# Kernel optimization log

Hardware: AMD Instinct MI355X
Metric: run time of the kernel (lower is better)

The kernel has to match this reference:

```python
import jax, jax.numpy as jnp
import numpy as np

D_MODEL = 1024
N_HEADS = 16
D_HEAD = D_MODEL // N_HEADS          # 64
ROT_DIM = D_HEAD // 2                # 32, rotary dim (lucidrains dim arg)
THETA = 10000.0
BATCH, SEQ = 4, 4096


def _rope(t):
    """lucidrains rotate_queries_or_keys with seq_dim=-2, applied to t of shape (H,B,dh,S).
    Positions run along the dh axis (size D_HEAD); rotation touches only the first
    ROT_DIM entries of the last axis (S); the rest passes through unchanged."""
    inv_freq = 1.0 / (THETA ** (jnp.arange(0, ROT_DIM, 2, dtype=jnp.float32) / ROT_DIM))  # (ROT_DIM//2,)
    pos = jnp.arange(D_HEAD, dtype=jnp.float32)                                           # (dh,)
    freqs = pos[:, None] * inv_freq[None, :]                                              # (dh, ROT_DIM//2)
    freqs = jnp.repeat(freqs, 2, axis=-1)                                                 # (dh, ROT_DIM) interleaved f0,f0,f1,f1
    cos, sin = jnp.cos(freqs), jnp.sin(freqs)                                             # broadcast over (H,B,dh,ROT_DIM)
    t_rot, t_pass = t[..., :ROT_DIM], t[..., ROT_DIM:]
    x1, x2 = t_rot[..., 0::2], t_rot[..., 1::2]
    rot_half = jnp.stack((-x2, x1), axis=-1).reshape(t_rot.shape)                         # rotate_half (adjacent pairs)
    t_rot = t_rot * cos + rot_half * sin
    return jnp.concatenate([t_rot, t_pass], axis=-1)


def setup_inputs() -> dict:
    key = jax.random.key(0)
    k1, k2, k3 = jax.random.split(key, 3)
    x = jax.random.normal(k1, (BATCH, SEQ, D_MODEL), jnp.float32)
    W = jax.random.normal(k2, (3 * D_MODEL, D_MODEL), jnp.float32) * (D_MODEL ** -0.5)  # torch Linear weight layout
    b = jax.random.normal(k3, (3 * D_MODEL,), jnp.float32) * 0.01
    return {"x": x, "W": W, "b": b}


def reference(x, W, b):
    B, S, _ = x.shape
    qkv = x @ W.T + b                                            # (B,S,3D)
    qkv = qkv.reshape(B, S, N_HEADS, 3 * D_HEAD).transpose(2, 0, 3, 1)  # (H,B,3dh,S)
    q, k, v = jnp.split(qkv, 3, axis=-2)                         # each (H,B,dh,S)
    q = _rope(q)
    k = _rope(k)
    scale = D_HEAD ** -0.5
    scores = jnp.einsum('hbds,hbes->hbde', q, k) * scale         # (H,B,dh,dh) — contracts over S
    probs = jax.nn.softmax(scores, axis=-1)
    out = jnp.einsum('hbde,hbes->hbds', probs, v)                # (H,B,dh,S)
    out = out.transpose(0, 2, 1, 3).reshape(B, S, N_HEADS * D_HEAD)  # faithful to torch transpose(1,2).reshape
    return out
```

## Files before the change

kernel.cpp:

```cpp
#include <hip/hip_runtime.h>
#include <stdint.h>

#define D_MODEL 1024
#define N_HEADS 16
#define D_HEAD  64
#define BATCH   4
#define SEQ     4096
#define BS      (BATCH*SEQ)
#define QKV_N   (3*D_MODEL)
#define HB      (N_HEADS*BATCH)
#define NCHUNK  8
#define CH_S    (SEQ/NCHUNK)

using f16x8 = __attribute__((ext_vector_type(8))) _Float16;
using f32x4 = __attribute__((ext_vector_type(4))) float;

__device__ static inline ushort f2h(float f) {
    _Float16 h = (_Float16)f; ushort u; __builtin_memcpy(&u, &h, 2); return u;
}
__device__ static inline float h2f(ushort u) {
    _Float16 h; __builtin_memcpy(&h, &u, 2); return (float)h;
}
__device__ static inline void async16(const ushort* g, ushort* l) {
    __builtin_amdgcn_global_load_lds(
        (const __attribute__((address_space(1))) void*)g,
        (__attribute__((address_space(3))) void*)l, 16, 0, 0);
}

__global__ __launch_bounds__(256)
void cvt_both(const float* __restrict__ x, const float* __restrict__ W,
              ushort* __restrict__ xh, ushort* __restrict__ Wh, int nx)
{
    int i = (blockIdx.x * 256 + threadIdx.x) * 8;
    const float* src; ushort* dst; int o;
    if (i < nx) { src = x; dst = xh; o = i; }
    else        { src = W; dst = Wh; o = i - nx; }
    float4 a = *(const float4*)(src + o);
    float4 b = *(const float4*)(src + o + 4);
    *(ushort4*)(dst + o)     = make_ushort4(f2h(a.x),f2h(a.y),f2h(a.z),f2h(a.w));
    *(ushort4*)(dst + o + 4) = make_ushort4(f2h(b.x),f2h(b.y),f2h(b.z),f2h(b.w));
}

__global__ __launch_bounds__(256)
void qkv_gemm_f16(const ushort* __restrict__ Ah, const ushort* __restrict__ Bh,
                  const float* __restrict__ bias,
                  ushort* __restrict__ qh, ushort* __restrict__ kh,
                  ushort* __restrict__ varr)
{
    __shared__ ushort sA[128 * 32];
    __shared__ ushort sB[128 * 32];
    const int t = threadIdx.x;
    const int lane = t & 63, w = t >> 6;
    const int m0 = blockIdx.y * 128, n0 = blockIdx.x * 128;

    const int ar0 = (w*2 + 0) * 16 + (lane >> 2);
    const int ar1 = (w*2 + 1) * 16 + (lane >> 2);
    const int kc  = (lane & 3) * 8;
    const ushort* gA0 = Ah + (size_t)(m0 + ar0) * D_MODEL + kc;
    const ushort* gA1 = Ah + (size_t)(m0 + ar1) * D_MODEL + kc;
    const ushort* gB0 = Bh + (size_t)(n0 + ar0) * D_MODEL + kc;
    const ushort* gB1 = Bh + (size_t)(n0 + ar1) * D_MODEL + kc;
    ushort* lA0 = &sA[(w*2 + 0) * 512];
    ushort* lA1 = &sA[(w*2 + 1) * 512];
    ushort* lB0 = &sB[(w*2 + 0) * 512];
    ushort* lB1 = &sB[(w*2 + 1) * 512];

    const int wm = (w >> 1) * 64, wn = (w & 1) * 64;
    const int fr = lane & 15, fq = (lane >> 4) * 8;

    f32x4 acc[4][4] = {};

    for (int k0 = 0; k0 < D_MODEL; k0 += 32) {
        __syncthreads();
        async16(gA0, lA0); async16(gA1, lA1);
        async16(gB0, lB0); async16(gB1, lB1);
        gA0 += 32; gA1 += 32; gB0 += 32; gB1 += 32;
        __syncthreads();

        f16x8 af[4], bf[4];
        #pragma unroll
        for (int i = 0; i < 4; ++i)
            af[i] = *(const f16x8*)&sA[(wm + i*16 + fr) * 32 + fq];
        #pragma unroll
        for (int j = 0; j < 4; ++j)
            bf[j] = *(const f16x8*)&sB[(wn + j*16 + fr) * 32 + fq];
        #pragma unroll
        for (int i = 0; i < 4; ++i)
            #pragma unroll
            for (int j = 0; j < 4; ++j)
                acc[i][j] = __builtin_amdgcn_mfma_f32_16x16x32_f16(
                                af[i], bf[j], acc[i][j], 0, 0, 0);
    }

    const int col = lane & 15, rq = (lane >> 4) * 4;
    const int cgb  = n0 + wn;
    const int h    = cgb / 192;
    const int type = (cgb % 192) / 64;
    const int b    = m0 >> 12;
    const int sb   = (m0 & 4095) + wm;

    if (type < 2) {
        ushort* dst = type ? kh : qh;
        #pragma unroll
        for (int j = 0; j < 4; ++j) {
            const int ci = j*16 + col;
            const float bj = bias[cgb + ci];
            const size_t rowoff = ((size_t)(h*4 + b)*64 + ci) * SEQ;
            #pragma unroll
            for (int i = 0; i < 4; ++i) {
                const int s0 = sb + i*16 + rq;
                float v0 = acc[i][j][0] + bj, v1 = acc[i][j][1] + bj;
                float v2 = acc[i][j][2] + bj, v3 = acc[i][j][3] + bj;
                if (s0 < 32) {
                    int mp = s0 >> 1;
                    float if0 = powf(10000.0f, -(float)mp / 16.0f);
                    float if1 = powf(10000.0f, -(float)(mp + 1) / 16.0f);
                    float a0 = (float)ci * if0, a1 = (float)ci * if1;
                    float c0 = cosf(a0), s0n = sinf(a0);
                    float c1 = cosf(a1), s1n = sinf(a1);
                    float n0 = v0*c0 - v1*s0n, n1 = v1*c0 + v0*s0n;
                    float n2 = v2*c1 - v3*s1n, n3 = v3*c1 + v2*s1n;
                    v0 = n0; v1 = n1; v2 = n2; v3 = n3;
                }
                *(ushort4*)&dst[rowoff + s0] = make_ushort4(
                    f2h(v0), f2h(v1), f2h(v2), f2h(v3));
            }
        }
    } else {
        #pragma unroll
        for (int j = 0; j < 4; ++j) {
            const int ci = j*16 + col;
            const float bj = bias[cgb + ci];
            #pragma unroll
            for (int i = 0; i < 4; ++i) {
                const int s0 = sb + i*16 + rq;
                #pragma unroll
                for (int r = 0; r < 4; ++r)
                    varr[((size_t)(h*4 + b)*SEQ + s0 + r)*64 + ci] =
                        f2h(acc[i][j][r] + bj);
            }
        }
    }
}

__global__ __launch_bounds__(256)
void scores_partial(const ushort* __restrict__ qh, const ushort* __restrict__ kh,
                    float* __restrict__ partial)
{
    __shared__ float L[4 * 4096];
    const int t = threadIdx.x, lane = t & 63, w = t >> 6;
    const int hb = blockIdx.x, chunk = blockIdx.y;
    const ushort* qb = qh + (size_t)hb * 64 * SEQ;
    const ushort* kb = kh + (size_t)hb * 64 * SEQ;
    const int fr = lane & 15, fq = (lane >> 4) * 8;

    f32x4 acc[4][4] = {};
    const int kbase = chunk * CH_S + w * (CH_S / 4);
    for (int kk = 0; kk < CH_S / 4; kk += 32) {
        const int k0 = kbase + kk;
        f16x8 af[4], bf[4];
        #pragma unroll
        for (int i = 0; i < 4; ++i)
            af[i] = *(const f16x8*)&qb[(size_t)(i*16 + fr) * SEQ + k0 + fq];
        #pragma unroll
        for (int j = 0; j < 4; ++j)
            bf[j] = *(const f16x8*)&kb[(size_t)(j*16 + fr) * SEQ + k0 + fq];
        #pragma unroll
        for (int i = 0; i < 4; ++i)
            #pragma unroll
            for (int j = 0; j < 4; ++j)
                acc[i][j] = __builtin_amdgcn_mfma_f32_16x16x32_f16(
                                af[i], bf[j], acc[i][j], 0, 0, 0);
    }

    float* Lw = &L[w * 4096];
    const int col = lane & 15, rq = (lane >> 4) * 4;
    #pragma unroll
    for (int i = 0; i < 4; ++i)
        #pragma unroll
        for (int j = 0; j < 4; ++j)
            #pragma unroll
            for (int r = 0; r < 4; ++r)
                Lw[(i*16 + rq + r)*64 + j*16 + col] = acc[i][j][r];
    __syncthreads();

    float* pb = partial + ((size_t)hb * NCHUNK + chunk) * 4096;
    #pragma unroll
    for (int u = 0; u < 4; ++u) {
        int idx = u*1024 + t*4;
        f32x4 s = *(f32x4*)&L[idx];
        s += *(f32x4*)&L[4096 + idx];
        s += *(f32x4*)&L[8192 + idx];
        s += *(f32x4*)&L[12288 + idx];
        *(f32x4*)&pb[idx] = s;
    }
}

__global__ __launch_bounds__(256)
void softmax_k(const float* __restrict__ partial, ushort* __restrict__ Pt)
{
    __shared__ float L[64 * 65];
    const int t = threadIdx.x;
    const int hb = blockIdx.x;
    const float* pb = partial + (size_t)hb * NCHUNK * 4096;

    #pragma unroll
    for (int u = 0; u < 16; ++u) {
        int idx = u*256 + t;
        float s = 0.f;
        #pragma unroll
        for (int c = 0; c < NCHUNK; ++c) s += pb[c*4096 + idx];
        L[(idx >> 6) * 65 + (idx & 63)] = s;
    }
    __syncthreads();

    if (t < 64) {
        float* row = &L[t * 65];
        float mx = -1e30f;
        for (int e = 0; e < 64; ++e) mx = fmaxf(mx, row[e]);
        float sum = 0.f;
        for (int e = 0; e < 64; ++e) {
            float v = expf(0.125f * (row[e] - mx));
            row[e] = v; sum += v;
        }
        float inv = 1.f / sum;
        ushort* pd = Pt + (size_t)hb * 4096 + t * 64;
        for (int e = 0; e < 64; ++e) pd[e] = f2h(row[e] * inv);
    }
}

__global__ __launch_bounds__(256)
void attn_out_mfma(const ushort* __restrict__ varr, const ushort* __restrict__ Pt,
                   float* __restrict__ out)
{
    const int t = threadIdx.x, lane = t & 63, w = t >> 6;
    const int hb = blockIdx.x;
    const int sb = blockIdx.y * 256 + w * 64;
    const int fr = lane & 15, fq = (lane >> 4) * 8;

    const ushort* Pb = Pt + (size_t)hb * 4096;
    const ushort* vb = varr + (size_t)hb * SEQ * 64;

    f16x8 aV[4][2], bP[4][2];
    #pragma unroll
    for (int i = 0; i < 4; ++i)
        #pragma unroll
        for (int ks = 0; ks < 2; ++ks)
            aV[i][ks] = *(const f16x8*)&vb[(size_t)(sb + i*16 + fr)*64 + ks*32 + fq];
    #pragma unroll
    for (int j = 0; j < 4; ++j)
        #pragma unroll
        for (int ks = 0; ks < 2; ++ks)
            bP[j][ks] = *(const f16x8*)&Pb[(j*16 + fr)*64 + ks*32 + fq];

    f32x4 acc[4][4] = {};
    #pragma unroll
    for (int ks = 0; ks < 2; ++ks)
        #pragma unroll
        for (int i = 0; i < 4; ++i)
            #pragma unroll
            for (int j = 0; j < 4; ++j)
                acc[i][j] = __builtin_amdgcn_mfma_f32_16x16x32_f16(
                                aV[i][ks], bP[j][ks], acc[i][j], 0, 0, 0);

    const int col = lane & 15, rq = (lane >> 4) * 4;
    const int h = hb >> 2, b = hb & 3;
    #pragma unroll
    for (int i = 0; i < 4; ++i)
        #pragma unroll
        for (int j = 0; j < 4; ++j) {
            const int dg = j*16 + col;
            size_t off = (((size_t)h*64 + dg)*4 + b)*SEQ + sb + i*16 + rq;
            *(float4*)&out[off] = make_float4(acc[i][j][0], acc[i][j][1],
                                              acc[i][j][2], acc[i][j][3]);
        }
}

extern "C" void kernel_launch(void* const* d_in, const int* in_sizes, int n_in,
                              void* d_out, int out_size, void* d_ws, size_t ws_size,
                              hipStream_t stream)
{
    const float* x    = (const float*)d_in[0];
    const float* W    = (const float*)d_in[1];
    const float* bias = (const float*)d_in[2];
    float* out = (float*)d_out;

    char* p = (char*)d_ws;
    ushort* qh   = (ushort*)p;  p += (size_t)HB * 64 * SEQ * 2;
    ushort* kh   = (ushort*)p;  p += (size_t)HB * 64 * SEQ * 2;
    ushort* varr = (ushort*)p;  p += (size_t)HB * SEQ * 64 * 2;
    ushort* Pth  = (ushort*)p;  p += (size_t)HB * 4096 * 2;
    float* partial = (float*)p; p += (size_t)HB * NCHUNK * 4096 * 4;
    ushort* xh   = (ushort*)p;  p += (size_t)BS * D_MODEL * 2;
    ushort* Wh   = (ushort*)p;  p += (size_t)QKV_N * D_MODEL * 2;

    const int nx = BS * D_MODEL;
    const int nw = QKV_N * D_MODEL;
    cvt_both<<<(nx + nw)/2048, 256, 0, stream>>>(x, W, xh, Wh, nx);

    qkv_gemm_f16<<<dim3(QKV_N/128, BS/128), 256, 0, stream>>>(
        xh, Wh, bias, qh, kh, varr);

    scores_partial<<<dim3(HB, NCHUNK), 256, 0, stream>>>(qh, kh, partial);
    softmax_k<<<HB, 256, 0, stream>>>(partial, Pth);
    attn_out_mfma<<<dim3(HB, 16), 256, 0, stream>>>(varr, Pth, out);
}
```

Measured before the change: 318.9 us.

## Rewrite QKV GEMM with 256x256 tiles, multi-stage async LDS pipeline and swizzle

Replaces the 128x128 single-buffered QKV GEMM with a 256x256-tile, 512-thread kernel. Each wave computes a 128x64 output from XOR-swizzled LDS and a four-stage async global-to-LDS pipeline whose loads are issued ahead of the MFMA phases. It also adds block-ID remapping for L2 locality, uses s_setprio around the MFMA bursts, and for V tiles swaps the MFMA operand order so the V output can be stored as vectorized ushort4. The goal is to hide global load latency, cut LDS bank conflicts and raise data reuse, at the cost of far more LDS (128 KB per block) and more registers per thread, which limit occupancy.

```diff
diff --git a/kernel.cpp b/kernel.cpp
--- a/kernel.cpp
+++ b/kernel.cpp
@@ -41,103 +41,170 @@
     *(ushort4*)(dst + o + 4) = make_ushort4(f2h(b.x),f2h(b.y),f2h(b.z),f2h(b.w));
 }
 
-__global__ __launch_bounds__(256)
+#define MF(a,b,c) __builtin_amdgcn_mfma_f32_16x16x32_f16(a,b,c,0,0,0)
+#define FENCE asm volatile("" ::: "memory")
+#define VM4 asm volatile("s_waitcnt vmcnt(4)" ::: "memory")
+#define VM0 asm volatile("s_waitcnt vmcnt(0)" ::: "memory")
+#define VMN do {} while (0)
+#define NOSTAGE do {} while (0)
+
+#define STAGE(CH, S0, S1, KC) do { \
+    async16((S0) + (KC), &lds[(CH)*8192 + d0]); \
+    async16((S1) + (KC), &lds[(CH)*8192 + d1]); } while (0)
+
+#define MROW(AI, I) \
+    acc[(I)*4+0]=MF(AI,b0,acc[(I)*4+0]); \
+    acc[(I)*4+1]=MF(AI,b1,acc[(I)*4+1]); \
+    acc[(I)*4+2]=MF(AI,b2,acc[(I)*4+2]); \
+    acc[(I)*4+3]=MF(AI,b3,acc[(I)*4+3]);
+
+#define MROWS(AI, I) \
+    acc[(I)*4+0]=MF(b0,AI,acc[(I)*4+0]); \
+    acc[(I)*4+1]=MF(b1,AI,acc[(I)*4+1]); \
+    acc[(I)*4+2]=MF(b2,AI,acc[(I)*4+2]); \
+    acc[(I)*4+3]=MF(b3,AI,acc[(I)*4+3]);
+
+#define PHASE(CA, CB, IH, STG, VMW) do { \
+    const ushort* pa = &lds[(CA)*8192 + aoff]; \
+    const ushort* pb = &lds[(CB)*8192 + boff]; \
+    f16x8 a0 = *(const f16x8*)(pa + ((IH)*4+0)*512); \
+    f16x8 a1 = *(const f16x8*)(pa + ((IH)*4+1)*512); \
+    f16x8 a2 = *(const f16x8*)(pa + ((IH)*4+2)*512); \
+    f16x8 a3 = *(const f16x8*)(pa + ((IH)*4+3)*512); \
+    f16x8 b0 = *(const f16x8*)(pb + 0*512); \
+    f16x8 b1 = *(const f16x8*)(pb + 1*512); \
+    f16x8 b2 = *(const f16x8*)(pb + 2*512); \
+    f16x8 b3 = *(const f16x8*)(pb + 3*512); \
+    STG; \
+    FENCE; __builtin_amdgcn_s_barrier(); FENCE; \
+    __builtin_amdgcn_s_setprio(1); \
+    if (!isV) { \
+        MROW(a0,(IH)*4+0) MROW(a1,(IH)*4+1) MROW(a2,(IH)*4+2) MROW(a3,(IH)*4+3) \
+    } else { \
+        MROWS(a0,(IH)*4+0) MROWS(a1,(IH)*4+1) MROWS(a2,(IH)*4+2) MROWS(a3,(IH)*4+3) \
+    } \
+    __builtin_amdgcn_s_setprio(0); \
+    asm volatile("s_waitcnt lgkmcnt(0)" ::: "memory"); \
+    VMW; \
+    FENCE; __builtin_amdgcn_s_barrier(); FENCE; \
+  } while (0)
+
+__global__ __launch_bounds__(512, 2)
 void qkv_gemm_f16(const ushort* __restrict__ Ah, const ushort* __restrict__ Bh,
                   const float* __restrict__ bias,
                   ushort* __restrict__ qh, ushort* __restrict__ kh,
                   ushort* __restrict__ varr)
 {
-    __shared__ ushort sA[128 * 32];
-    __shared__ ushort sB[128 * 32];
+    __shared__ ushort lds[8 * 8192];
     const int t = threadIdx.x;
     const int lane = t & 63, w = t >> 6;
-    const int m0 = blockIdx.y * 128, n0 = blockIdx.x * 128;
-
-    const int ar0 = (w*2 + 0) * 16 + (lane >> 2);
-    const int ar1 = (w*2 + 1) * 16 + (lane >> 2);
-    const int kc  = (lane & 3) * 8;
-    const ushort* gA0 = Ah + (size_t)(m0 + ar0) * D_MODEL + kc;
-    const ushort* gA1 = Ah + (size_t)(m0 + ar1) * D_MODEL + kc;
-    const ushort* gB0 = Bh + (size_t)(n0 + ar0) * D_MODEL + kc;
-    const ushort* gB1 = Bh + (size_t)(n0 + ar1) * D_MODEL + kc;
-    ushort* lA0 = &sA[(w*2 + 0) * 512];
-    ushort* lA1 = &sA[(w*2 + 1) * 512];
-    ushort* lB0 = &sB[(w*2 + 0) * 512];
-    ushort* lB1 = &sB[(w*2 + 1) * 512];
-
-    const int wm = (w >> 1) * 64, wn = (w & 1) * 64;
-    const int fr = lane & 15, fq = (lane >> 4) * 8;
-
-    f32x4 acc[4][4] = {};
-
-    for (int k0 = 0; k0 < D_MODEL; k0 += 32) {
-        __syncthreads();
-        async16(gA0, lA0); async16(gA1, lA1);
-        async16(gB0, lB0); async16(gB1, lB1);
-        gA0 += 32; gA1 += 32; gB0 += 32; gB1 += 32;
-        __syncthreads();
-
-        f16x8 af[4], bf[4];
-        #pragma unroll
-        for (int i = 0; i < 4; ++i)
-            af[i] = *(const f16x8*)&sA[(wm + i*16 + fr) * 32 + fq];
-        #pragma unroll
-        for (int j = 0; j < 4; ++j)
-            bf[j] = *(const f16x8*)&sB[(wn + j*16 + fr) * 32 + fq];
-        #pragma unroll
-        for (int i = 0; i < 4; ++i)
-            #pragma unroll
-            for (int j = 0; j < 4; ++j)
-                acc[i][j] = __builtin_amdgcn_mfma_f32_16x16x32_f16(
-                                af[i], bf[j], acc[i][j], 0, 0, 0);
-    }
+
+    const int id0 = blockIdx.y * 12 + blockIdx.x;
+    const int ids = (id0 & 7) * 96 + (id0 >> 3);
+    const int n0 = (ids % 12) * 256;
+    const int m0 = (ids / 12) * 256;
+
+    const int wm = (w >> 2) * 128;
+    const int wn = (w & 3) * 64;
+    const int fr = lane & 15;
+    const int hq = lane >> 4;
+
+    const int u0 = t, u1 = 512 + t;
+    const int rp0 = u0 >> 3, rp1 = u1 >> 3;
+    const int sl0 = (u0 & 7) ^ (rp0 & 7), sl1 = (u1 & 7) ^ (rp1 & 7);
+    const int r0 = rp0 * 2 + (sl0 >> 2), r1 = rp1 * 2 + (sl1 >> 2);
+    const int c0 = (sl0 & 3) * 8,        c1 = (sl1 & 3) * 8;
+    const ushort* aS0 = Ah + (size_t)(m0 + r0) * D_MODEL + c0;
+    const ushort* aS1 = Ah + (size_t)(m0 + r1) * D_MODEL + c1;
+    const ushort* bS0 = Bh + (size_t)(n0 + r0) * D_MODEL + c0;
+    const ushort* bS1 = Bh + (size_t)(n0 + r1) * D_MODEL + c1;
+    const int d0 = w * 512;
+    const int d1 = 4096 + w * 512;
+
+    const int rdo  = ((fr >> 1) * 64) + ((((fr & 1) * 4 + hq) ^ ((fr >> 1) & 7)) * 8);
+    const int aoff = wm * 32 + rdo;
+    const int boff = wn * 32 + rdo;
+
+    const int cgb = n0 + wn;
+    const int typ = __builtin_amdgcn_readfirstlane((cgb % 192) / 64);
+    const bool isV = (typ == 2);
+
+    f32x4 acc[32] = {};
+
+    STAGE(0, aS0, aS1, 0);
+    STAGE(2, bS0, bS1, 0);
+    STAGE(1, aS0, aS1, 32);
+    STAGE(3, bS0, bS1, 32);
+    STAGE(4, aS0, aS1, 64);
+    STAGE(6, bS0, bS1, 64);
+    VM4;
+    __builtin_amdgcn_s_barrier();
+    FENCE;
+
+    #pragma unroll 1
+    for (int it = 0; it < 7; ++it) {
+        const int kb = it * 128;
+        PHASE(0,2,0, STAGE(5, aS0,aS1, kb+96),  VMN);
+        PHASE(0,2,1, STAGE(7, bS0,bS1, kb+96),  VMN);
+        PHASE(1,3,0, STAGE(0, aS0,aS1, kb+128), VMN);
+        PHASE(1,3,1, STAGE(2, bS0,bS1, kb+128), VM4);
+        PHASE(4,6,0, STAGE(1, aS0,aS1, kb+160), VMN);
+        PHASE(4,6,1, STAGE(3, bS0,bS1, kb+160), VMN);
+        PHASE(5,7,0, STAGE(4, aS0,aS1, kb+192), VMN);
+        PHASE(5,7,1, STAGE(6, bS0,bS1, kb+192), VM4);
+    }
+    PHASE(0,2,0, STAGE(5, aS0,aS1, 992), VMN);
+    PHASE(0,2,1, STAGE(7, bS0,bS1, 992), VMN);
+    PHASE(1,3,0, NOSTAGE, VMN);
+    PHASE(1,3,1, NOSTAGE, VM0);
+    PHASE(4,6,0, NOSTAGE, VMN);
+    PHASE(4,6,1, NOSTAGE, VMN);
+    PHASE(5,7,0, NOSTAGE, VMN);
+    PHASE(5,7,1, NOSTAGE, VMN);
 
     const int col = lane & 15, rq = (lane >> 4) * 4;
-    const int cgb  = n0 + wn;
-    const int h    = cgb / 192;
-    const int type = (cgb % 192) / 64;
-    const int b    = m0 >> 12;
-    const int sb   = (m0 & 4095) + wm;
-
-    if (type < 2) {
-        ushort* dst = type ? kh : qh;
+    const int h   = cgb / 192;
+    const int b   = m0 >> 12;
+    const int sbl = (m0 & 4095) + wm;
+
+    if (typ < 2) {
+        ushort* dst = typ ? kh : qh;
         #pragma unroll
         for (int j = 0; j < 4; ++j) {
             const int ci = j*16 + col;
             const float bj = bias[cgb + ci];
             const size_t rowoff = ((size_t)(h*4 + b)*64 + ci) * SEQ;
             #pragma unroll
-            for (int i = 0; i < 4; ++i) {
-                const int s0 = sb + i*16 + rq;
-                float v0 = acc[i][j][0] + bj, v1 = acc[i][j][1] + bj;
-                float v2 = acc[i][j][2] + bj, v3 = acc[i][j][3] + bj;
+            for (int i = 0; i < 8; ++i) {
+                const int s0 = sbl + i*16 + rq;
+                float v0 = acc[i*4+j][0] + bj, v1 = acc[i*4+j][1] + bj;
+                float v2 = acc[i*4+j][2] + bj, v3 = acc[i*4+j][3] + bj;
                 if (s0 < 32) {
                     int mp = s0 >> 1;
                     float if0 = powf(10000.0f, -(float)mp / 16.0f);
                     float if1 = powf(10000.0f, -(float)(mp + 1) / 16.0f);
                     float a0 = (float)ci * if0, a1 = (float)ci * if1;
-                    float c0 = cosf(a0), s0n = sinf(a0);
-                    float c1 = cosf(a1), s1n = sinf(a1);
-                    float n0 = v0*c0 - v1*s0n, n1 = v1*c0 + v0*s0n;
-                    float n2 = v2*c1 - v3*s1n, n3 = v3*c1 + v2*s1n;
-                    v0 = n0; v1 = n1; v2 = n2; v3 = n3;
+                    float cc0 = cosf(a0), s0n = sinf(a0);
+                    float cc1 = cosf(a1), s1n = sinf(a1);
+                    float n0_ = v0*cc0 - v1*s0n, n1_ = v1*cc0 + v0*s0n;
+                    float n2_ = v2*cc1 - v3*s1n, n3_ = v3*cc1 + v2*s1n;
+                    v0 = n0_; v1 = n1_; v2 = n2_; v3 = n3_;
                 }
                 *(ushort4*)&dst[rowoff + s0] = make_ushort4(
                     f2h(v0), f2h(v1), f2h(v2), f2h(v3));
             }
         }
     } else {
+        const size_t base = (size_t)(h*4 + b) * SEQ;
         #pragma unroll
         for (int j = 0; j < 4; ++j) {
-            const int ci = j*16 + col;
-            const float bj = bias[cgb + ci];
-            #pragma unroll
-            for (int i = 0; i < 4; ++i) {
-                const int s0 = sb + i*16 + rq;
-                #pragma unroll
-                for (int r = 0; r < 4; ++r)
-                    varr[((size_t)(h*4 + b)*SEQ + s0 + r)*64 + ci] =
-                        f2h(acc[i][j][r] + bj);
+            const float4 b4 = *(const float4*)&bias[cgb + j*16 + rq];
+            #pragma unroll
+            for (int i = 0; i < 8; ++i) {
+                const int s = sbl + i*16 + col;
+                *(ushort4*)&varr[(base + s)*64 + j*16 + rq] = make_ushort4(
+                    f2h(acc[i*4+j][0] + b4.x), f2h(acc[i*4+j][1] + b4.y),
+                    f2h(acc[i*4+j][2] + b4.z), f2h(acc[i*4+j][3] + b4.w));
             }
         }
     }
@@ -298,7 +365,7 @@
     const int nw = QKV_N * D_MODEL;
     cvt_both<<<(nx + nw)/2048, 256, 0, stream>>>(x, W, xh, Wh, nx);
 
-    qkv_gemm_f16<<<dim3(QKV_N/128, BS/128), 256, 0, stream>>>(
+    qkv_gemm_f16<<<dim3(QKV_N/256, BS/256), 512, 0, stream>>>(
         xh, Wh, bias, qh, kh, varr);
 
     scores_partial<<<dim3(HB, NCHUNK), 256, 0, stream>>>(qh, kh, partial);
```

New measurement: 442.9 us. 1.39x slower.
